# Optimization experiments

Measured on AMD Instinct MI355X. Metric: run time of the kernel, lower is better.

Reference implementation:

```python
import jax, jax.numpy as jnp
import numpy as np

B, S, E = 2048, 23, 768
RED, H, NUM_LABELS = 256, 8, 25
DH = RED // H
DELTA = 0.1
EPS_LN = 1e-5


def setup_inputs() -> dict:
    key = jax.random.key(0)
    ks = jax.random.split(key, 20)
    g = lambda k, shape, fan: jax.random.normal(k, shape, dtype=jnp.float32) * (1.0 / np.sqrt(fan))
    inp = {
        'cls_embeddings': jax.random.normal(ks[0], (B, S, E), dtype=jnp.float32),
        'existing_mask': jax.random.randint(ks[1], (B, S), 0, 2, dtype=jnp.int32),
        'missing_emb': g(ks[2], (S, E), E),
        'W1': g(ks[3], (E // 2, E), E), 'b1': jnp.zeros((E // 2,), jnp.float32),
        'W2': g(ks[4], (RED, E // 2), E // 2), 'b2': jnp.zeros((RED,), jnp.float32),
        'ln_g': jnp.ones((RED,), jnp.float32), 'ln_b': jnp.zeros((RED,), jnp.float32),
        'Wq': g(ks[5], (RED, RED), RED), 'bq': jnp.zeros((RED,), jnp.float32),
        'Wk': g(ks[6], (RED, RED), RED), 'bk': jnp.zeros((RED,), jnp.float32),
        'Wv': g(ks[7], (RED, RED), RED), 'bv': jnp.zeros((RED,), jnp.float32),
        'Wo': g(ks[8], (RED, RED), RED), 'bo': jnp.zeros((RED,), jnp.float32),
        'Wp': g(ks[9], (NUM_LABELS, RED), RED), 'bp': jnp.zeros((NUM_LABELS,), jnp.float32),
    }
    return inp


def _layer_norm(x, g, b):
    mu = jnp.mean(x, axis=-1, keepdims=True)
    var = jnp.mean(jnp.square(x - mu), axis=-1, keepdims=True)
    return (x - mu) * jax.lax.rsqrt(var + EPS_LN) * g + b


def _forward(cls_embeddings, existing_mask, missing_emb, W1, b1, W2, b2, ln_g, ln_b,
             Wq, bq, Wk, bk, Wv, bv, Wo, bo, Wp, bp):
    exist = existing_mask > 0                              # [B,S] bool
    # Gather: existing sections use BERT CLS, missing slots use learned embeddings
    sec = jnp.where(exist[..., None], cls_embeddings, missing_emb[None])  # [B,S,E]
    # SectionDimReducer (exact-erf GELU as in nn.GELU default)
    h = jax.nn.gelu(sec @ W1.T + b1, approximate=False)
    h = jax.nn.gelu(h @ W2.T + b2, approximate=False)
    red = _layer_norm(h, ln_g, ln_b)                       # [B,S,RED]
    # Tiny MHA: every slot queries the existing sections of its own EHR
    q = (red @ Wq.T + bq).reshape(B, S, H, DH)
    k = (red @ Wk.T + bk).reshape(B, S, H, DH)
    v = (red @ Wv.T + bv).reshape(B, S, H, DH)
    scores = jnp.einsum('bqhd,bkhd->bhqk', q, k) / np.sqrt(DH)
    scores = jnp.where(exist[:, None, None, :], scores, -1e9)
    attn = jax.nn.softmax(scores, axis=-1)                 # [B,H,S,S]
    ctx = jnp.einsum('bhqk,bkhd->bqhd', attn, v).reshape(B, S, RED)
    mha_out = ctx @ Wo.T + bo                              # [B,S,RED]
    # Scatter: only missing slots (of EHRs with >=1 existing section) are replaced
    any_exist = jnp.any(exist, axis=1)                     # [B]
    use_attn = (~exist) & any_exist[:, None]               # [B,S]
    updated = jnp.where(use_attn[..., None], mha_out, red)
    # margin-based orthogonality loss on section embeddings
    norm = updated / jnp.maximum(jnp.linalg.norm(updated, axis=-1, keepdims=True), 1e-8)
    gram = jnp.einsum('bid,bjd->bij', norm, norm)          # [B,S,S]
    off = 1.0 - jnp.eye(S, dtype=updated.dtype)
    loss_orth = jnp.sum(jax.nn.relu(jnp.abs(gram) - DELTA) * off) / (B * S * (S - 1))
    logits = updated.mean(axis=1) @ Wp.T + bp              # [B,NUM_LABELS]
    return loss_orth, logits


def reference(cls_embeddings, existing_mask, missing_emb, W1, b1, W2, b2, ln_g, ln_b,
              Wq, bq, Wk, bk, Wv, bv, Wo, bo, Wp, bp):
    return _forward(cls_embeddings, existing_mask, missing_emb, W1, b1, W2, b2, ln_g, ln_b,
                    Wq, bq, Wk, bk, Wv, bv, Wo, bo, Wp, bp)
```

## Files before the change

kernel.cpp:

```cpp
#include <hip/hip_runtime.h>

typedef unsigned short u16;
typedef unsigned int u32;
typedef __attribute__((ext_vector_type(8))) short short8;
typedef __attribute__((ext_vector_type(4))) float f32x4;

struct __align__(8) us4 { u16 x, y, z, w; };

__device__ __forceinline__ float bf1(u16 v){ return __uint_as_float(((u32)v) << 16); }
__device__ __forceinline__ float bflo(u32 u){ return __uint_as_float(u << 16); }
__device__ __forceinline__ float bfhi(u32 u){ return __uint_as_float(u & 0xFFFF0000u); }
__device__ __forceinline__ u16 fbf(float f){
    u32 u = __float_as_uint(f);
    return (u16)((u + 0x7FFFu + ((u >> 16) & 1u)) >> 16);
}
__device__ __forceinline__ float gelu_exact(float x){
    return 0.5f * x * (1.0f + erff(x * 0.70710678118654752f));
}
__device__ __forceinline__ void unp8(uint4 u, float* f){
    f[0]=bflo(u.x); f[1]=bfhi(u.x); f[2]=bflo(u.y); f[3]=bfhi(u.y);
    f[4]=bflo(u.z); f[5]=bfhi(u.z); f[6]=bflo(u.w); f[7]=bfhi(u.w);
}
__device__ __forceinline__ uint4 pack8(float4 a, float4 b){
    uint4 u;
    u.x = (u32)fbf(a.x) | ((u32)fbf(a.y) << 16);
    u.y = (u32)fbf(a.z) | ((u32)fbf(a.w) << 16);
    u.z = (u32)fbf(b.x) | ((u32)fbf(b.y) << 16);
    u.w = (u32)fbf(b.z) | ((u32)fbf(b.w) << 16);
    return u;
}


__global__ __launch_bounds__(256) void wconv(
    const float* __restrict__ W1, const float* __restrict__ W2,
    const float* __restrict__ Wq, const float* __restrict__ Wk,
    const float* __restrict__ Wv, const float* __restrict__ Wo,
    const float* __restrict__ Wp, u16* __restrict__ dst)
{
    const int i = blockIdx.x * 256 + threadIdx.x;
    const float* s; int o;
    if      (i < 294912) { s = W1; o = i; }
    else if (i < 393216) { s = W2; o = i - 294912; }
    else if (i < 458752) { s = Wq; o = i - 393216; }
    else if (i < 524288) { s = Wk; o = i - 458752; }
    else if (i < 589824) { s = Wv; o = i - 524288; }
    else if (i < 655360) { s = Wo; o = i - 589824; }
    else                 { s = Wp; o = i - 655360; }
    dst[i] = fbf(s[o]);
}

__global__ __launch_bounds__(256) void gemm1_kernel(
    const float* __restrict__ cls, const int* __restrict__ mask,
    const float* __restrict__ missing, const u16* __restrict__ W,
    const float* __restrict__ bias, u16* __restrict__ C)
{
    const int K = 768, M = 384;
    __shared__ u16 As[128 * 40];
    __shared__ u16 Bs[128 * 40];
    const int tid = threadIdx.x;
    const int w = tid >> 6, lane = tid & 63;
    const int nBase = blockIdx.y * 128, mBase = blockIdx.x * 128;
    const int wr = w >> 1, wc = w & 1;
    const int r0 = tid >> 2;
    const int co = (tid & 3) * 8;
    const int frow = lane & 15, quad = lane >> 4;

    const int rowA0 = nBase + r0, rowA1 = nBase + r0 + 64;
    const float* ap0 = (mask[rowA0] > 0) ? cls + (size_t)rowA0 * 768
                                         : missing + (size_t)(rowA0 % 23) * 768;
    const float* ap1 = (mask[rowA1] > 0) ? cls + (size_t)rowA1 * 768
                                         : missing + (size_t)(rowA1 % 23) * 768;
    const u16* bp0 = W + (size_t)(mBase + r0) * K;
    const u16* bp1 = W + (size_t)(mBase + r0 + 64) * K;

    f32x4 acc[4][4];
#pragma unroll
    for (int mt = 0; mt < 4; ++mt)
#pragma unroll
        for (int nt = 0; nt < 4; ++nt) acc[mt][nt] = f32x4{0.f, 0.f, 0.f, 0.f};

    float4 a0a = *(const float4*)(ap0 + co), a0b = *(const float4*)(ap0 + co + 4);
    float4 a1a = *(const float4*)(ap1 + co), a1b = *(const float4*)(ap1 + co + 4);
    uint4 pb0 = *(const uint4*)(bp0 + co), pb1 = *(const uint4*)(bp1 + co);

    for (int k0 = 0; k0 < K; k0 += 32) {
        __syncthreads();
        *(uint4*)(As + r0 * 40 + co) = pack8(a0a, a0b);
        *(uint4*)(As + (r0 + 64) * 40 + co) = pack8(a1a, a1b);
        *(uint4*)(Bs + r0 * 40 + co) = pb0;
        *(uint4*)(Bs + (r0 + 64) * 40 + co) = pb1;
        __syncthreads();
        if (k0 + 32 < K) {
            const int kn = k0 + 32 + co;
            a0a = *(const float4*)(ap0 + kn); a0b = *(const float4*)(ap0 + kn + 4);
            a1a = *(const float4*)(ap1 + kn); a1b = *(const float4*)(ap1 + kn + 4);
            pb0 = *(const uint4*)(bp0 + kn);  pb1 = *(const uint4*)(bp1 + kn);
        }
        short8 af[4], bfv[4];
#pragma unroll
        for (int mt = 0; mt < 4; ++mt)
            af[mt] = *(const short8*)(As + (wr * 64 + mt * 16 + frow) * 40 + quad * 8);
#pragma unroll
        for (int nt = 0; nt < 4; ++nt)
            bfv[nt] = *(const short8*)(Bs + (wc * 64 + nt * 16 + frow) * 40 + quad * 8);
#pragma unroll
        for (int mt = 0; mt < 4; ++mt)
#pragma unroll
            for (int nt = 0; nt < 4; ++nt)
                acc[mt][nt] = __builtin_amdgcn_mfma_f32_16x16x32_bf16(
                    af[mt], bfv[nt], acc[mt][nt], 0, 0, 0);
    }

#pragma unroll
    for (int nt = 0; nt < 4; ++nt) {
        const int col = mBase + wc * 64 + nt * 16 + frow;
        const float bv = bias[col];
#pragma unroll
        for (int mt = 0; mt < 4; ++mt)
#pragma unroll
            for (int reg = 0; reg < 4; ++reg) {
                const int row = nBase + wr * 64 + mt * 16 + quad * 4 + reg;
                C[(size_t)row * M + col] = fbf(gelu_exact(acc[mt][nt][reg] + bv));
            }
    }
}

__global__ __launch_bounds__(256) void gemm_bt(
    const u16* __restrict__ A, const u16* __restrict__ W,
    const float* __restrict__ bias, u16* __restrict__ C, int K, int M)
{
    __shared__ u16 As[128 * 40];
    __shared__ u16 Bs[128 * 40];
    const int tid = threadIdx.x;
    const int w = tid >> 6, lane = tid & 63;
    const int nBase = blockIdx.y * 128, mBase = blockIdx.x * 128;
    const int wr = w >> 1, wc = w & 1;
    const int r0 = tid >> 2;
    const int co = (tid & 3) * 8;
    const int frow = lane & 15, quad = lane >> 4;

    f32x4 acc[4][4];
#pragma unroll
    for (int mt = 0; mt < 4; ++mt)
#pragma unroll
        for (int nt = 0; nt < 4; ++nt) acc[mt][nt] = f32x4{0.f, 0.f, 0.f, 0.f};

    uint4 pa0 = *(const uint4*)(A + (size_t)(nBase + r0) * K + co);
    uint4 pa1 = *(const uint4*)(A + (size_t)(nBase + r0 + 64) * K + co);
    uint4 pb0 = *(const uint4*)(W + (size_t)(mBase + r0) * K + co);
    uint4 pb1 = *(const uint4*)(W + (size_t)(mBase + r0 + 64) * K + co);

    for (int k0 = 0; k0 < K; k0 += 32) {
        __syncthreads();
        *(uint4*)(As + r0 * 40 + co) = pa0;
        *(uint4*)(As + (r0 + 64) * 40 + co) = pa1;
        *(uint4*)(Bs + r0 * 40 + co) = pb0;
        *(uint4*)(Bs + (r0 + 64) * 40 + co) = pb1;
        __syncthreads();
        if (k0 + 32 < K) {
            const int kn = k0 + 32 + co;
            pa0 = *(const uint4*)(A + (size_t)(nBase + r0) * K + kn);
            pa1 = *(const uint4*)(A + (size_t)(nBase + r0 + 64) * K + kn);
            pb0 = *(const uint4*)(W + (size_t)(mBase + r0) * K + kn);
            pb1 = *(const uint4*)(W + (size_t)(mBase + r0 + 64) * K + kn);
        }
        short8 af[4], bfv[4];
#pragma unroll
        for (int mt = 0; mt < 4; ++mt)
            af[mt] = *(const short8*)(As + (wr * 64 + mt * 16 + frow) * 40 + quad * 8);
#pragma unroll
        for (int nt = 0; nt < 4; ++nt)
            bfv[nt] = *(const short8*)(Bs + (wc * 64 + nt * 16 + frow) * 40 + quad * 8);
#pragma unroll
        for (int mt = 0; mt < 4; ++mt)
#pragma unroll
            for (int nt = 0; nt < 4; ++nt)
                acc[mt][nt] = __builtin_amdgcn_mfma_f32_16x16x32_bf16(
                    af[mt], bfv[nt], acc[mt][nt], 0, 0, 0);
    }

#pragma unroll
    for (int nt = 0; nt < 4; ++nt) {
        const int col = mBase + wc * 64 + nt * 16 + frow;
        const float bv = bias[col];
#pragma unroll
        for (int mt = 0; mt < 4; ++mt)
#pragma unroll
            for (int reg = 0; reg < 4; ++reg) {
                const int row = nBase + wr * 64 + mt * 16 + quad * 4 + reg;
                C[(size_t)row * M + col] = fbf(gelu_exact(acc[mt][nt][reg] + bv));
            }
    }
}

__global__ __launch_bounds__(256) void ln_kernel(
    u16* __restrict__ X, const float* __restrict__ g, const float* __restrict__ b)
{
    const int w = threadIdx.x >> 6, lane = threadIdx.x & 63;
    const size_t row = (size_t)blockIdx.x * 4 + w;
    u16* xp = X + row * 256 + lane * 4;
    us4 uv = *(const us4*)xp;
    float x0 = bf1(uv.x), x1 = bf1(uv.y), x2 = bf1(uv.z), x3 = bf1(uv.w);
    float s = x0 + x1 + x2 + x3;
#pragma unroll
    for (int m = 32; m; m >>= 1) s += __shfl_xor(s, m);
    const float mu = s * (1.f / 256.f);
    const float d0 = x0 - mu, d1 = x1 - mu, d2 = x2 - mu, d3 = x3 - mu;
    float vs = d0 * d0 + d1 * d1 + d2 * d2 + d3 * d3;
#pragma unroll
    for (int m = 32; m; m >>= 1) vs += __shfl_xor(vs, m);
    const float rs = rsqrtf(vs * (1.f / 256.f) + 1e-5f);
    const float4 gv = *(const float4*)(g + lane * 4);
    const float4 bv = *(const float4*)(b + lane * 4);
    us4 o;
    o.x = fbf(d0 * rs * gv.x + bv.x);
    o.y = fbf(d1 * rs * gv.y + bv.y);
    o.z = fbf(d2 * rs * gv.z + bv.z);
    o.w = fbf(d3 * rs * gv.w + bv.w);
    *(us4*)xp = o;
}

#define QSTR 264
__global__ __launch_bounds__(256) void attn1_kernel(
    u16* __restrict__ redb, const int* __restrict__ mask,
    const u16* __restrict__ Wqkvb,
    const float* __restrict__ bq, const float* __restrict__ bk,
    const float* __restrict__ bv, const u16* __restrict__ Wob,
    const float* __restrict__ bo)
{
    __shared__ __align__(16) unsigned char SM[44768];
    u16* s_rq = (u16*)SM;
    u16* s_k  = (u16*)(SM + 12144);
    u16* s_vT = (u16*)(SM + 24288);
    __shared__ int sEx[23];
    __shared__ int sMiss[23];
    __shared__ float sMaskF[32];

    const int b = blockIdx.x, t = threadIdx.x;
    const int w = t >> 6, lane = t & 63;
    const int frow = lane & 15, quad = lane >> 4;
    const int r0c = frow;
    const int r1c = (16 + frow > 22) ? 22 : 16 + frow;

    if (t < 23) sEx[t] = mask[b * 23 + t];
    __syncthreads();
    if (t == 0) {
        int any = 0;
        for (int s = 0; s < 23; ++s) any |= (sEx[s] > 0) ? 1 : 0;
        for (int s = 0; s < 23; ++s) sMiss[s] = (any && sEx[s] <= 0) ? 1 : 0;
    }
    if (t < 32) sMaskF[t] = (t < 23 && sEx[t] > 0) ? 0.f : -1e9f;
    for (int i = t; i < 1280; i += 256) ((uint4*)s_vT)[i] = make_uint4(0u, 0u, 0u, 0u);
    for (int i = t; i < 736; i += 256) {
        const int s = i >> 5, c8 = (i & 31) * 8;
        *(uint4*)(s_rq + s * QSTR + c8) =
            *(const uint4*)(redb + ((size_t)(b * 23 + s)) * 256 + c8);
    }
    __syncthreads();

    {
        f32x4 qacc[2][12];
#pragma unroll
        for (int mt = 0; mt < 2; ++mt)
#pragma unroll
            for (int nt = 0; nt < 12; ++nt) qacc[mt][nt] = f32x4{0.f, 0.f, 0.f, 0.f};
        for (int k0 = 0; k0 < 256; k0 += 32) {
            short8 a0 = *(const short8*)(s_rq + r0c * QSTR + k0 + quad * 8);
            short8 a1 = *(const short8*)(s_rq + r1c * QSTR + k0 + quad * 8);
#pragma unroll
            for (int nt = 0; nt < 12; ++nt) {
                const int n = w * 192 + nt * 16 + frow;
                short8 bfr = *(const short8*)(Wqkvb + (size_t)n * 256 + k0 + quad * 8);
                qacc[0][nt] = __builtin_amdgcn_mfma_f32_16x16x32_bf16(a0, bfr, qacc[0][nt], 0, 0, 0);
                qacc[1][nt] = __builtin_amdgcn_mfma_f32_16x16x32_bf16(a1, bfr, qacc[1][nt], 0, 0, 0);
            }
        }
        __syncthreads();
#pragma unroll
        for (int mt = 0; mt < 2; ++mt)
#pragma unroll
            for (int nt = 0; nt < 12; ++nt) {
                const int col = w * 192 + nt * 16 + frow;
                const int seg = col >> 8, cm = col & 255;
                const float bb = (seg == 0) ? bq[cm] : (seg == 1) ? bk[cm] : bv[cm];
#pragma unroll
                for (int reg = 0; reg < 4; ++reg) {
                    const int s = mt * 16 + quad * 4 + reg;
                    if (s < 23) {
                        const u16 hv = fbf(qacc[mt][nt][reg] + bb);
                        if (seg == 0)      s_rq[s * QSTR + cm] = hv;
                        else if (seg == 1) s_k[s * QSTR + cm] = hv;
                        else               s_vT[cm * 40 + s] = hv;
                    }
                }
            }
    }
    __syncthreads();

    {
        const float scl = 0.17677669529663687f;
        const float m0 = sMaskF[frow];
        const float m1 = sMaskF[16 + frow];
        const f32x4 z4 = f32x4{0.f, 0.f, 0.f, 0.f};
#pragma unroll
        for (int hh2 = 0; hh2 < 2; ++hh2) {
            const int hb = (w * 2 + hh2) * 32;
            short8 aq0 = *(const short8*)(s_rq + r0c * QSTR + hb + quad * 8);
            short8 aq1 = *(const short8*)(s_rq + r1c * QSTR + hb + quad * 8);
            short8 bk0 = *(const short8*)(s_k + r0c * QSTR + hb + quad * 8);
            short8 bk1 = *(const short8*)(s_k + r1c * QSTR + hb + quad * 8);
            f32x4 s00 = __builtin_amdgcn_mfma_f32_16x16x32_bf16(aq0, bk0, z4, 0, 0, 0);
            f32x4 s01 = __builtin_amdgcn_mfma_f32_16x16x32_bf16(aq0, bk1, z4, 0, 0, 0);
            f32x4 s10 = __builtin_amdgcn_mfma_f32_16x16x32_bf16(aq1, bk0, z4, 0, 0, 0);
            f32x4 s11 = __builtin_amdgcn_mfma_f32_16x16x32_bf16(aq1, bk1, z4, 0, 0, 0);
#pragma unroll
            for (int mt = 0; mt < 2; ++mt) {
                f32x4& c0 = mt ? s10 : s00;
                f32x4& c1 = mt ? s11 : s01;
#pragma unroll
                for (int reg = 0; reg < 4; ++reg) {
                    float v0 = c0[reg] * scl + m0;
                    float v1 = c1[reg] * scl + m1;
                    float mx = fmaxf(v0, v1);
#pragma unroll
                    for (int m = 8; m; m >>= 1) mx = fmaxf(mx, __shfl_xor(mx, m));
                    float p0 = __expf(v0 - mx), p1 = __expf(v1 - mx);
                    float sm = p0 + p1;
#pragma unroll
                    for (int m = 8; m; m >>= 1) sm += __shfl_xor(sm, m);
                    const float inv = 1.f / sm;
                    c0[reg] = p0 * inv;
                    c1[reg] = p1 * inv;
                }
            }
#pragma unroll
            for (int reg = 0; reg < 4; ++reg) {
                const int q0r = quad * 4 + reg;
                s_k[q0r * QSTR + hb + frow]      = fbf(s00[reg]);
                s_k[q0r * QSTR + hb + 16 + frow] = fbf(s01[reg]);
                const int q1r = 16 + quad * 4 + reg;
                if (q1r < 23) {
                    s_k[q1r * QSTR + hb + frow]      = fbf(s10[reg]);
                    s_k[q1r * QSTR + hb + 16 + frow] = fbf(s11[reg]);
                }
            }
            short8 pa0 = *(const short8*)(s_k + r0c * QSTR + hb + quad * 8);
            short8 pa1 = *(const short8*)(s_k + r1c * QSTR + hb + quad * 8);
            short8 bv0 = *(const short8*)(s_vT + (hb + frow) * 40 + quad * 8);
            short8 bv1 = *(const short8*)(s_vT + (hb + 16 + frow) * 40 + quad * 8);
            f32x4 c00 = __builtin_amdgcn_mfma_f32_16x16x32_bf16(pa0, bv0, z4, 0, 0, 0);
            f32x4 c01 = __builtin_amdgcn_mfma_f32_16x16x32_bf16(pa0, bv1, z4, 0, 0, 0);
            f32x4 c10 = __builtin_amdgcn_mfma_f32_16x16x32_bf16(pa1, bv0, z4, 0, 0, 0);
            f32x4 c11 = __builtin_amdgcn_mfma_f32_16x16x32_bf16(pa1, bv1, z4, 0, 0, 0);
#pragma unroll
            for (int reg = 0; reg < 4; ++reg) {
                const int q0r = quad * 4 + reg;
                s_rq[q0r * QSTR + hb + frow]      = fbf(c00[reg]);
                s_rq[q0r * QSTR + hb + 16 + frow] = fbf(c01[reg]);
                const int q1r = 16 + quad * 4 + reg;
                if (q1r < 23) {
                    s_rq[q1r * QSTR + hb + frow]      = fbf(c10[reg]);
                    s_rq[q1r * QSTR + hb + 16 + frow] = fbf(c11[reg]);
                }
            }
        }
    }
    __syncthreads();

    {
        f32x4 wacc[2][4];
#pragma unroll
        for (int mt = 0; mt < 2; ++mt)
#pragma unroll
            for (int nt = 0; nt < 4; ++nt) wacc[mt][nt] = f32x4{0.f, 0.f, 0.f, 0.f};
        for (int k0 = 0; k0 < 256; k0 += 32) {
            short8 a0 = *(const short8*)(s_rq + r0c * QSTR + k0 + quad * 8);
            short8 a1 = *(const short8*)(s_rq + r1c * QSTR + k0 + quad * 8);
#pragma unroll
            for (int nt = 0; nt < 4; ++nt) {
                const int n = w * 64 + nt * 16 + frow;
                short8 bfr = *(const short8*)(Wob + (size_t)n * 256 + k0 + quad * 8);
                wacc[0][nt] = __builtin_amdgcn_mfma_f32_16x16x32_bf16(a0, bfr, wacc[0][nt], 0, 0, 0);
                wacc[1][nt] = __builtin_amdgcn_mfma_f32_16x16x32_bf16(a1, bfr, wacc[1][nt], 0, 0, 0);
            }
        }
#pragma unroll
        for (int mt = 0; mt < 2; ++mt)
#pragma unroll
            for (int nt = 0; nt < 4; ++nt) {
                const int col = w * 64 + nt * 16 + frow;
                const float bvv = bo[col];
#pragma unroll
                for (int reg = 0; reg < 4; ++reg) {
                    const int s = mt * 16 + quad * 4 + reg;
                    if (s < 23 && sMiss[s])
                        redb[((size_t)(b * 23 + s)) * 256 + col] =
                            fbf(wacc[mt][nt][reg] + bvv);
                }
            }
    }
}

__global__ __launch_bounds__(256) void tail_kernel(
    const u16* __restrict__ redb, const u16* __restrict__ Wpb,
    const float* __restrict__ bp, float* __restrict__ out,
    float* __restrict__ lossAcc)
{
    __shared__ __align__(16) u16 s_u[23 * QSTR];
    __shared__ float sInv[23];
    __shared__ float sPool[256];
    __shared__ float sRsc[4];

    const int b = blockIdx.x, t = threadIdx.x;
    const int w = t >> 6, lane = t & 63;

    for (int i = t; i < 736; i += 256) {
        const int s = i >> 5, c8 = (i & 31) * 8;
        *(uint4*)(s_u + s * QSTR + c8) =
            *(const uint4*)(redb + ((size_t)(b * 23 + s)) * 256 + c8);
    }
    __syncthreads();

    if (t < 23) {
        float ss = 0.f;
        for (int c8 = 0; c8 < 32; ++c8) {
            float rf[8]; unp8(*(const uint4*)(s_u + t * QSTR + c8 * 8), rf);
#pragma unroll
            for (int e = 0; e < 8; ++e) ss += rf[e] * rf[e];
        }
        sInv[t] = 1.f / fmaxf(sqrtf(ss), 1e-8f);
    }
    __syncthreads();

    {
        float contrib = 0.f;
        if (t < 253) {
            int i = 0, rem = t, cnt = 22;
            while (rem >= cnt) { rem -= cnt; --cnt; ++i; }
            const int j = i + 1 + rem;
            float dp = 0.f;
            for (int c8 = 0; c8 < 32; ++c8) {
                float fa[8], fb[8];
                unp8(*(const uint4*)(s_u + i * QSTR + c8 * 8), fa);
                unp8(*(const uint4*)(s_u + j * QSTR + c8 * 8), fb);
#pragma unroll
                for (int e = 0; e < 8; ++e) dp += fa[e] * fb[e];
            }
            const float g = dp * sInv[i] * sInv[j];
            const float c = fabsf(g) - 0.1f;
            contrib = (c > 0.f) ? 2.f * c : 0.f;
        }
#pragma unroll
        for (int m = 32; m; m >>= 1) contrib += __shfl_xor(contrib, m);
        if (lane == 0) sRsc[w] = contrib;
        __syncthreads();
        if (t == 0) atomicAdd(lossAcc, sRsc[0] + sRsc[1] + sRsc[2] + sRsc[3]);
    }

    {
        float pv = 0.f;
#pragma unroll
        for (int s = 0; s < 23; ++s) pv += bf1(s_u[s * QSTR + t]);
        sPool[t] = pv * (1.f / 23.f);
    }
    __syncthreads();
    if (t < 25) {
        float a = bp[t];
        for (int c8 = 0; c8 < 32; ++c8) {
            float wf[8]; unp8(*(const uint4*)(Wpb + (size_t)t * 256 + c8 * 8), wf);
            const float4 p0 = *(const float4*)(sPool + c8 * 8);
            const float4 p1 = *(const float4*)(sPool + c8 * 8 + 4);
            a += wf[0] * p0.x + wf[1] * p0.y + wf[2] * p0.z + wf[3] * p0.w
               + wf[4] * p1.x + wf[5] * p1.y + wf[6] * p1.z + wf[7] * p1.w;
        }
        out[1 + b * 25 + t] = a;
    }
}

__global__ void loss_finalize(const float* __restrict__ lossAcc, float* __restrict__ out)
{
    out[0] = lossAcc[0] * (1.f / 1036288.f);
}

extern "C" void kernel_launch(void* const* d_in, const int* in_sizes, int n_in,
                              void* d_out, int out_size, void* d_ws, size_t ws_size,
                              hipStream_t stream)
{
    const float* cls     = (const float*)d_in[0];
    const int*   mask    = (const int*)d_in[1];
    const float* missing = (const float*)d_in[2];
    const float* W1 = (const float*)d_in[3];  const float* b1 = (const float*)d_in[4];
    const float* W2 = (const float*)d_in[5];  const float* b2 = (const float*)d_in[6];
    const float* lng = (const float*)d_in[7]; const float* lnb = (const float*)d_in[8];
    const float* Wq = (const float*)d_in[9];  const float* bq = (const float*)d_in[10];
    const float* Wk = (const float*)d_in[11]; const float* bk = (const float*)d_in[12];
    const float* Wv = (const float*)d_in[13]; const float* bv = (const float*)d_in[14];
    const float* Wo = (const float*)d_in[15]; const float* bo = (const float*)d_in[16];
    const float* Wp = (const float*)d_in[17]; const float* bp = (const float*)d_in[18];
    float* out = (float*)d_out;

    char* ws = (char*)d_ws;
    u16* h1b  = (u16*)ws;
    u16* redb = (u16*)(ws + 36175872);
    u16* Wb   = (u16*)(ws + 60293120);
    u16* W1b   = Wb;
    u16* W2b   = Wb + 294912;
    u16* Wqkvb = Wb + 393216;
    u16* Wob   = Wb + 589824;
    u16* Wpb   = Wb + 655360;
    float* lossAcc = (float*)(ws + 61616640);

    hipMemsetAsync(lossAcc, 0, sizeof(float), stream);

    wconv<<<2585, 256, 0, stream>>>(W1, W2, Wq, Wk, Wv, Wo, Wp, Wb);
    gemm1_kernel<<<dim3(3, 368), 256, 0, stream>>>(cls, mask, missing, W1b, b1, h1b);
    gemm_bt<<<dim3(2, 368), 256, 0, stream>>>(h1b, W2b, b2, redb, 384, 256);
    ln_kernel<<<11776, 256, 0, stream>>>(redb, lng, lnb);
    attn1_kernel<<<2048, 256, 0, stream>>>(redb, mask, Wqkvb, bq, bk, bv, Wob, bo);
    tail_kernel<<<2048, 256, 0, stream>>>(redb, Wpb, bp, out, lossAcc);
    loss_finalize<<<1, 1, 0, stream>>>(lossAcc, out);
}
```

Measured before the change: 593.9 us.

## Fuse attention and tail kernels, keeping updated embeddings in shared memory

Merges the attention kernel and the orthogonality-loss/pooling tail kernel into one kernel per EHR. The updated section embeddings are assembled in shared memory (the MHA output for missing slots, with redb reloaded for the other slots) instead of being written back to global memory and read again. It also reorders the QKV column assignment so each wave computes its own heads' Q, K and V without a block barrier, replaces the serial mask scan with a ballot, and shrinks the V-transpose stride. Shared memory is reused across phases to fit the fused kernel, which adds aliasing risk.

```diff
diff --git a/kernel.cpp b/kernel.cpp
--- a/kernel.cpp
+++ b/kernel.cpp
@@ -221,20 +221,24 @@
 }
 
 #define QSTR 264
-__global__ __launch_bounds__(256) void attn1_kernel(
-    u16* __restrict__ redb, const int* __restrict__ mask,
+__global__ __launch_bounds__(256) void attn_tail_kernel(
+    const u16* __restrict__ redb, const int* __restrict__ mask,
     const u16* __restrict__ Wqkvb,
     const float* __restrict__ bq, const float* __restrict__ bk,
     const float* __restrict__ bv, const u16* __restrict__ Wob,
-    const float* __restrict__ bo)
-{
-    __shared__ __align__(16) unsigned char SM[44768];
+    const float* __restrict__ bo, const u16* __restrict__ Wpb,
+    const float* __restrict__ bp, float* __restrict__ out,
+    float* __restrict__ lossAcc)
+{
+    __shared__ __align__(16) unsigned char SM[40960];
     u16* s_rq = (u16*)SM;
     u16* s_k  = (u16*)(SM + 12144);
     u16* s_vT = (u16*)(SM + 24288);
-    __shared__ int sEx[23];
-    __shared__ int sMiss[23];
-    __shared__ float sMaskF[32];
+    int* sEx   = (int*)(SM + 40672);
+    int* sMiss = (int*)(SM + 40764);
+    float* sInv  = (float*)(SM + 24288);
+    float* sPool = (float*)(SM + 24384);
+    float* sRsc  = (float*)(SM + 25472);
 
     const int b = blockIdx.x, t = threadIdx.x;
     const int w = t >> 6, lane = t & 63;
@@ -242,15 +246,15 @@
     const int r0c = frow;
     const int r1c = (16 + frow > 22) ? 22 : 16 + frow;
 
-    if (t < 23) sEx[t] = mask[b * 23 + t];
-    __syncthreads();
-    if (t == 0) {
-        int any = 0;
-        for (int s = 0; s < 23; ++s) any |= (sEx[s] > 0) ? 1 : 0;
-        for (int s = 0; s < 23; ++s) sMiss[s] = (any && sEx[s] <= 0) ? 1 : 0;
-    }
-    if (t < 32) sMaskF[t] = (t < 23 && sEx[t] > 0) ? 0.f : -1e9f;
-    for (int i = t; i < 1280; i += 256) ((uint4*)s_vT)[i] = make_uint4(0u, 0u, 0u, 0u);
+    {
+        const int myEx = (t < 23) ? mask[b * 23 + t] : 0;
+        if (t < 23) sEx[t] = myEx;
+        if (t < 64) {
+            const unsigned long long ball = __ballot((t < 23) && (myEx > 0));
+            if (t < 23) sMiss[t] = (ball != 0ull && myEx <= 0) ? 1 : 0;
+        }
+    }
+    for (int i = t; i < 1024; i += 256) ((uint4*)s_vT)[i] = make_uint4(0u, 0u, 0u, 0u);
     for (int i = t; i < 736; i += 256) {
         const int s = i >> 5, c8 = (i & 31) * 8;
         *(uint4*)(s_rq + s * QSTR + c8) =
@@ -269,7 +273,7 @@
             short8 a1 = *(const short8*)(s_rq + r1c * QSTR + k0 + quad * 8);
 #pragma unroll
             for (int nt = 0; nt < 12; ++nt) {
-                const int n = w * 192 + nt * 16 + frow;
+                const int n = (nt >> 2) * 256 + w * 64 + (nt & 3) * 16 + frow;
                 short8 bfr = *(const short8*)(Wqkvb + (size_t)n * 256 + k0 + quad * 8);
                 qacc[0][nt] = __builtin_amdgcn_mfma_f32_16x16x32_bf16(a0, bfr, qacc[0][nt], 0, 0, 0);
                 qacc[1][nt] = __builtin_amdgcn_mfma_f32_16x16x32_bf16(a1, bfr, qacc[1][nt], 0, 0, 0);
@@ -277,12 +281,12 @@
         }
         __syncthreads();
 #pragma unroll
-        for (int mt = 0; mt < 2; ++mt)
-#pragma unroll
-            for (int nt = 0; nt < 12; ++nt) {
-                const int col = w * 192 + nt * 16 + frow;
-                const int seg = col >> 8, cm = col & 255;
-                const float bb = (seg == 0) ? bq[cm] : (seg == 1) ? bk[cm] : bv[cm];
+        for (int nt = 0; nt < 12; ++nt) {
+            const int seg = nt >> 2;
+            const int cm = w * 64 + (nt & 3) * 16 + frow;
+            const float bb = (seg == 0) ? bq[cm] : (seg == 1) ? bk[cm] : bv[cm];
+#pragma unroll
+            for (int mt = 0; mt < 2; ++mt)
 #pragma unroll
                 for (int reg = 0; reg < 4; ++reg) {
                     const int s = mt * 16 + quad * 4 + reg;
@@ -290,21 +294,20 @@
                         const u16 hv = fbf(qacc[mt][nt][reg] + bb);
                         if (seg == 0)      s_rq[s * QSTR + cm] = hv;
                         else if (seg == 1) s_k[s * QSTR + cm] = hv;
-                        else               s_vT[cm * 40 + s] = hv;
+                        else               s_vT[cm * 32 + s] = hv;
                     }
                 }
-            }
-    }
-    __syncthreads();
+        }
+    }
 
     {
         const float scl = 0.17677669529663687f;
-        const float m0 = sMaskF[frow];
-        const float m1 = sMaskF[16 + frow];
+        const float m0 = (sEx[frow] > 0) ? 0.f : -1e9f;
+        const float m1 = (16 + frow < 23 && sEx[16 + frow] > 0) ? 0.f : -1e9f;
         const f32x4 z4 = f32x4{0.f, 0.f, 0.f, 0.f};
 #pragma unroll
         for (int hh2 = 0; hh2 < 2; ++hh2) {
-            const int hb = (w * 2 + hh2) * 32;
+            const int hb = w * 64 + hh2 * 32;
             short8 aq0 = *(const short8*)(s_rq + r0c * QSTR + hb + quad * 8);
             short8 aq1 = *(const short8*)(s_rq + r1c * QSTR + hb + quad * 8);
             short8 bk0 = *(const short8*)(s_k + r0c * QSTR + hb + quad * 8);
@@ -346,8 +349,8 @@
             }
             short8 pa0 = *(const short8*)(s_k + r0c * QSTR + hb + quad * 8);
             short8 pa1 = *(const short8*)(s_k + r1c * QSTR + hb + quad * 8);
-            short8 bv0 = *(const short8*)(s_vT + (hb + frow) * 40 + quad * 8);
-            short8 bv1 = *(const short8*)(s_vT + (hb + 16 + frow) * 40 + quad * 8);
+            short8 bv0 = *(const short8*)(s_vT + (hb + frow) * 32 + quad * 8);
+            short8 bv1 = *(const short8*)(s_vT + (hb + 16 + frow) * 32 + quad * 8);
             f32x4 c00 = __builtin_amdgcn_mfma_f32_16x16x32_bf16(pa0, bv0, z4, 0, 0, 0);
             f32x4 c01 = __builtin_amdgcn_mfma_f32_16x16x32_bf16(pa0, bv1, z4, 0, 0, 0);
             f32x4 c10 = __builtin_amdgcn_mfma_f32_16x16x32_bf16(pa1, bv0, z4, 0, 0, 0);
@@ -384,47 +387,34 @@
                 wacc[1][nt] = __builtin_amdgcn_mfma_f32_16x16x32_bf16(a1, bfr, wacc[1][nt], 0, 0, 0);
             }
         }
-#pragma unroll
-        for (int mt = 0; mt < 2; ++mt)
-#pragma unroll
-            for (int nt = 0; nt < 4; ++nt) {
-                const int col = w * 64 + nt * 16 + frow;
-                const float bvv = bo[col];
+        for (int i = t; i < 736; i += 256) {
+            const int s = i >> 5;
+            if (!sMiss[s]) {
+                const int c8 = (i & 31) * 8;
+                *(uint4*)(s_k + s * QSTR + c8) =
+                    *(const uint4*)(redb + ((size_t)(b * 23 + s)) * 256 + c8);
+            }
+        }
+#pragma unroll
+        for (int nt = 0; nt < 4; ++nt) {
+            const int col = w * 64 + nt * 16 + frow;
+            const float bvv = bo[col];
+#pragma unroll
+            for (int mt = 0; mt < 2; ++mt)
 #pragma unroll
                 for (int reg = 0; reg < 4; ++reg) {
                     const int s = mt * 16 + quad * 4 + reg;
                     if (s < 23 && sMiss[s])
-                        redb[((size_t)(b * 23 + s)) * 256 + col] =
-                            fbf(wacc[mt][nt][reg] + bvv);
+                        s_k[s * QSTR + col] = fbf(wacc[mt][nt][reg] + bvv);
                 }
-            }
-    }
-}
-
-__global__ __launch_bounds__(256) void tail_kernel(
-    const u16* __restrict__ redb, const u16* __restrict__ Wpb,
-    const float* __restrict__ bp, float* __restrict__ out,
-    float* __restrict__ lossAcc)
-{
-    __shared__ __align__(16) u16 s_u[23 * QSTR];
-    __shared__ float sInv[23];
-    __shared__ float sPool[256];
-    __shared__ float sRsc[4];
-
-    const int b = blockIdx.x, t = threadIdx.x;
-    const int w = t >> 6, lane = t & 63;
-
-    for (int i = t; i < 736; i += 256) {
-        const int s = i >> 5, c8 = (i & 31) * 8;
-        *(uint4*)(s_u + s * QSTR + c8) =
-            *(const uint4*)(redb + ((size_t)(b * 23 + s)) * 256 + c8);
+        }
     }
     __syncthreads();
 
     if (t < 23) {
         float ss = 0.f;
         for (int c8 = 0; c8 < 32; ++c8) {
-            float rf[8]; unp8(*(const uint4*)(s_u + t * QSTR + c8 * 8), rf);
+            float rf[8]; unp8(*(const uint4*)(s_k + t * QSTR + c8 * 8), rf);
 #pragma unroll
             for (int e = 0; e < 8; ++e) ss += rf[e] * rf[e];
         }
@@ -441,8 +431,8 @@
             float dp = 0.f;
             for (int c8 = 0; c8 < 32; ++c8) {
                 float fa[8], fb[8];
-                unp8(*(const uint4*)(s_u + i * QSTR + c8 * 8), fa);
-                unp8(*(const uint4*)(s_u + j * QSTR + c8 * 8), fb);
+                unp8(*(const uint4*)(s_k + i * QSTR + c8 * 8), fa);
+                unp8(*(const uint4*)(s_k + j * QSTR + c8 * 8), fb);
 #pragma unroll
                 for (int e = 0; e < 8; ++e) dp += fa[e] * fb[e];
             }
@@ -453,17 +443,15 @@
 #pragma unroll
         for (int m = 32; m; m >>= 1) contrib += __shfl_xor(contrib, m);
         if (lane == 0) sRsc[w] = contrib;
-        __syncthreads();
-        if (t == 0) atomicAdd(lossAcc, sRsc[0] + sRsc[1] + sRsc[2] + sRsc[3]);
-    }
-
-    {
+
         float pv = 0.f;
 #pragma unroll
-        for (int s = 0; s < 23; ++s) pv += bf1(s_u[s * QSTR + t]);
+        for (int s = 0; s < 23; ++s) pv += bf1(s_k[s * QSTR + t]);
         sPool[t] = pv * (1.f / 23.f);
     }
     __syncthreads();
+
+    if (t == 0) atomicAdd(lossAcc, sRsc[0] + sRsc[1] + sRsc[2] + sRsc[3]);
     if (t < 25) {
         float a = bp[t];
         for (int c8 = 0; c8 < 32; ++c8) {
@@ -516,7 +504,7 @@
     gemm1_kernel<<<dim3(3, 368), 256, 0, stream>>>(cls, mask, missing, W1b, b1, h1b);
     gemm_bt<<<dim3(2, 368), 256, 0, stream>>>(h1b, W2b, b2, redb, 384, 256);
     ln_kernel<<<11776, 256, 0, stream>>>(redb, lng, lnb);
-    attn1_kernel<<<2048, 256, 0, stream>>>(redb, mask, Wqkvb, bq, bk, bv, Wob, bo);
-    tail_kernel<<<2048, 256, 0, stream>>>(redb, Wpb, bp, out, lossAcc);
+    attn_tail_kernel<<<2048, 256, 0, stream>>>(redb, mask, Wqkvb, bq, bk, bv,
+                                               Wob, bo, Wpb, bp, out, lossAcc);
     loss_finalize<<<1, 1, 0, stream>>>(lossAcc, out);
 }
```

Result: faster. 564.0 us (-5.0%).
